# Performance work log

Hardware: AMD Instinct MI355X
Metric: run time of the kernel (lower is better)

Reference implementation:

```python
import jax, jax.numpy as jnp
import numpy as np

B, L, D, H, OUT = 4, 2048, 1024, 8, 256
DH = D // H
EPS = 1e-12


def setup_inputs() -> dict:
    key = jax.random.key(0)
    ks = jax.random.split(key, 20)
    s = lambda fan_in: 1.0 / np.sqrt(fan_in)
    def lin(k, fin, fout):
        k1, k2 = jax.random.split(k)
        w = jax.random.uniform(k1, (fin, fout), jnp.float32, -s(fin), s(fin))
        b = jax.random.uniform(k2, (fout,), jnp.float32, -s(fin), s(fin))
        return w, b
    x = jax.random.normal(ks[0], (B, L, D), jnp.float32)
    wq, bq = lin(ks[1], D, D)
    wk, bk = lin(ks[2], D, D)
    wv, bv = lin(ks[3], D, D)
    gamma = jnp.ones((D,), jnp.float32)
    beta = jnp.zeros((D,), jnp.float32)
    wff, bff = lin(ks[4], D, D)
    wc1, bc1 = lin(ks[5], D, D)
    wc2, bc2 = lin(ks[6], D, 1)
    wl1, bl1 = lin(ks[7], L, L)
    wl2, bl2 = lin(ks[8], L, OUT)
    return dict(x=x, wq=wq, bq=bq, wk=wk, bk=bk, wv=wv, bv=bv,
                gamma=gamma, beta=beta, wff=wff, bff=bff,
                wc1=wc1, bc1=bc1, wc2=wc2, bc2=bc2,
                wl1=wl1, bl1=bl1, wl2=wl2, bl2=bl2)


def layernorm(x, gamma, beta):
    mean = x.mean(-1, keepdims=True)
    var = ((x - mean) ** 2).mean(-1, keepdims=True)  # biased variance
    return gamma * (x - mean) / jnp.sqrt(var + EPS) + beta


def reference(x, wq, bq, wk, bk, wv, bv, gamma, beta, wff, bff,
              wc1, bc1, wc2, bc2, wl1, bl1, wl2, bl2):
    # multi-head self-attention (dropout = identity at inference)
    q = (x @ wq + bq).reshape(B, L, H, DH)
    k = (x @ wk + bk).reshape(B, L, H, DH)
    v = (x @ wv + bv).reshape(B, L, H, DH)
    scores = jnp.einsum('bqhd,bkhd->bhqk', q, k) / np.sqrt(DH)
    attn = jax.nn.softmax(scores, axis=-1)                  # [B,H,L,L]
    ctx = jnp.einsum('bhqk,bkhd->bqhd', attn, v).reshape(B, L, D)
    h = layernorm(x + ctx, gamma, beta)
    # feedforward: Linear + ReLU (hidden = d_model), residual + same layernorm params
    ff = jax.nn.relu(h @ wff + bff)
    h = layernorm(h + ff, gamma, beta)
    # collapse d_model -> 1
    c = jax.nn.relu(h @ wc1 + bc1)
    c = jax.nn.relu(c @ wc2 + bc2)                          # [B,L,1]
    c = jnp.squeeze(c, axis=-1)                             # [B,L]
    # collapse length -> out_featuresize
    c = jax.nn.relu(c @ wl1 + bl1)
    out = c @ wl2 + bl2                                     # [B,OUT]
    return out
```

## Files before the change

### kernel.cpp

```cpp
#include <hip/hip_runtime.h>

typedef unsigned short u16;
typedef unsigned int u32;
typedef __attribute__((ext_vector_type(4))) float f32x4;
typedef __attribute__((ext_vector_type(8))) short short8;
typedef __attribute__((ext_vector_type(4))) u32 u32x4;
typedef __attribute__((ext_vector_type(4))) u16 u16x4;

#define BB 4
#define LL 2048
#define DD 1024
#define HH 8
#define DHH 128

__device__ __forceinline__ u16 f2b(float f) {
  u32 u = __builtin_bit_cast(u32, f);
  u += 0x7fffu + ((u >> 16) & 1u);
  return (u16)(u >> 16);
}
__device__ __forceinline__ float b2f(u16 h) {
  u32 u = ((u32)h) << 16;
  return __builtin_bit_cast(float, u);
}
__device__ __forceinline__ float exp2_fast(float x) {
  float r;
  asm("v_exp_f32 %0, %1" : "=v"(r) : "v"(x));
  return r;
}
__device__ __forceinline__ u32 packbf(float a, float b) {
  return (u32)f2b(a) | ((u32)f2b(b) << 16);
}
__device__ __forceinline__ u32 bperm(int srcLane, u32 v) {
  return (u32)__builtin_amdgcn_ds_bpermute(srcLane << 2, (int)v);
}

#define GLDS16(g, l)                                                          \
  __builtin_amdgcn_global_load_lds(                                           \
      (const __attribute__((address_space(1))) void*)(g),                     \
      (__attribute__((address_space(3))) void*)(l), 16, 0, 0)

#define MFMA_BF16 __builtin_amdgcn_mfma_f32_16x16x32_bf16

__global__ __launch_bounds__(256) void cvt_k(const float* __restrict__ X,
                                             u16* __restrict__ Xb, long n) {
  long i = ((long)blockIdx.x * 256 + threadIdx.x) * 4;
  if (i >= n) return;
  f32x4 v = *(const f32x4*)(X + i);
  u16x4 o;
#pragma unroll
  for (int k = 0; k < 4; k++) o[k] = f2b(v[k]);
  *(u16x4*)(Xb + i) = o;
}

__global__ __launch_bounds__(256) void tr5_k(
    const float* __restrict__ s0, const float* __restrict__ s1,
    const float* __restrict__ s2, const float* __restrict__ s3,
    const float* __restrict__ s4, u16* __restrict__ d0, u16* __restrict__ d1,
    u16* __restrict__ d2, u16* __restrict__ d3, u16* __restrict__ d4) {
  const float* W;
  u16* WT;
  switch (blockIdx.z) {
    case 0: W = s0; WT = d0; break;
    case 1: W = s1; WT = d1; break;
    case 2: W = s2; WT = d2; break;
    case 3: W = s3; WT = d3; break;
    default: W = s4; WT = d4; break;
  }
  __shared__ float tile[32][33];
  const int bx = blockIdx.x, by = blockIdx.y;
  const int tx = threadIdx.x & 31, ty = threadIdx.x >> 5;
#pragma unroll
  for (int i = 0; i < 4; i++)
    tile[ty + i * 8][tx] =
        W[(long)(by * 32 + ty + i * 8) * 1024 + bx * 32 + tx];
  __syncthreads();
#pragma unroll
  for (int i = 0; i < 4; i++)
    WT[(long)(bx * 32 + ty + i * 8) * 1024 + by * 32 + tx] =
        f2b(tile[tx][ty + i * 8]);
}

__global__ __launch_bounds__(256, 3) void qkv_k(
    const u16* __restrict__ A, const u16* __restrict__ QT,
    const u16* __restrict__ KT, const u16* __restrict__ VTw,
    const float* __restrict__ bq, const float* __restrict__ bk,
    const float* __restrict__ bv, float qscale, u16* __restrict__ Qo,
    u16* __restrict__ Ko, u16* __restrict__ Vo) {
  __shared__ u16 As[2][128 * 32];
  __shared__ u16 Bs[2][128 * 32];
  const int K = 1024;
  const int nwg = gridDim.x * gridDim.y;
  const int bid = blockIdx.x + blockIdx.y * gridDim.x;
  const int swz = (bid & 7) * (nwg >> 3) + (bid >> 3);
  const int bxi = swz % 24, byi = swz / 24;
  const int sector = bxi >> 3;
  const u16* BT = sector == 0 ? QT : (sector == 1 ? KT : VTw);
  const float* bias = sector == 0 ? bq : (sector == 1 ? bk : bv);
  const float scale = sector == 0 ? qscale : 1.f;
  const int t = threadIdx.x;
  const int l = t & 63, w = t >> 6;
  const int lr = l & 15, lg = l >> 4;
  const int wr = (w >> 1) * 64, wc = (w & 1) * 64;
  const long bm = (long)byi * 128, bn = (long)(bxi & 7) * 128;
  const int srow = l >> 2;
  const int scol = (l & 3) * 8;
  const u16* Ag0 = A + (bm + w * 32 + srow) * (long)K + scol;
  const u16* Ag1 = A + (bm + w * 32 + 16 + srow) * (long)K + scol;
  const u16* Bg0 = BT + (bn + w * 32 + srow) * (long)K + scol;
  const u16* Bg1 = BT + (bn + w * 32 + 16 + srow) * (long)K + scol;
  const int wo = w * 1024;
  f32x4 acc[4][4] = {};
  GLDS16(Ag0, &As[0][wo]);
  GLDS16(Ag1, &As[0][wo + 512]);
  GLDS16(Bg0, &Bs[0][wo]);
  GLDS16(Bg1, &Bs[0][wo + 512]);
  __syncthreads();
  int cur = 0;
  for (int k0 = 0; k0 < K; k0 += 32) {
    const int nxt = cur ^ 1;
    if (k0 + 32 < K) {
      GLDS16(Ag0 + k0 + 32, &As[nxt][wo]);
      GLDS16(Ag1 + k0 + 32, &As[nxt][wo + 512]);
      GLDS16(Bg0 + k0 + 32, &Bs[nxt][wo]);
      GLDS16(Bg1 + k0 + 32, &Bs[nxt][wo + 512]);
    }
    short8 af[4], bf[4];
#pragma unroll
    for (int i = 0; i < 4; i++)
      af[i] = *(const short8*)&As[cur][(wr + i * 16 + lr) * 32 + lg * 8];
#pragma unroll
    for (int i = 0; i < 4; i++)
      bf[i] = *(const short8*)&Bs[cur][(wc + i * 16 + lr) * 32 + lg * 8];
#pragma unroll
    for (int i = 0; i < 4; i++)
#pragma unroll
      for (int j = 0; j < 4; j++)
        acc[i][j] = MFMA_BF16(af[i], bf[j], acc[i][j], 0, 0, 0);
    __syncthreads();
    cur = nxt;
  }
#pragma unroll
  for (int i = 0; i < 4; i++)
#pragma unroll
    for (int j = 0; j < 4; j++) {
      long col = bn + wc + j * 16 + lr;
      float bvv = bias[col];
      if (sector == 2) {
        long row0 = bm + wr + i * 16 + lg * 4;
        long b = row0 >> 11, l0 = row0 & 2047;
        u16x4 ov;
#pragma unroll
        for (int r = 0; r < 4; r++) ov[r] = f2b(acc[i][j][r] + bvv);
        *(u16x4*)(Vo + (b * 1024 + col) * 2048 + l0) = ov;
      } else {
        u16* Out = sector == 0 ? Qo : Ko;
#pragma unroll
        for (int r = 0; r < 4; r++) {
          long row = bm + wr + i * 16 + lg * 4 + r;
          Out[row * 1024 + col] = f2b((acc[i][j][r] + bvv) * scale);
        }
      }
    }
}

template <bool RELU, int OMODE>
__global__ __launch_bounds__(256, 4) void gemm_k(
    const u16* __restrict__ A, const u16* __restrict__ BT,
    const float* __restrict__ bias, u16* __restrict__ Cb,
    const float* __restrict__ w2, float* __restrict__ cvec, int M, int N,
    int K) {
  __shared__ u16 As[2][64 * 32];
  __shared__ u16 Bs[2][128 * 32];
  const int nwg = gridDim.x * gridDim.y;
  const int bid = blockIdx.x + blockIdx.y * gridDim.x;
  const int swz = (bid & 7) * (nwg >> 3) + (bid >> 3);
  const int bxi = swz % gridDim.x, byi = swz / gridDim.x;
  const int t = threadIdx.x;
  const int l = t & 63, w = t >> 6;
  const int lr = l & 15, lg = l >> 4;
  const int wr = (w >> 1) * 32, wc = (w & 1) * 64;
  const long bm = (long)byi * 64, bn = (long)bxi * 128;
  const int srow = l >> 2;
  const int scol = (l & 3) * 8;
  const u16* Ag0 = A + (bm + w * 16 + srow) * (long)K + scol;
  const u16* Bg0 = BT + (bn + w * 32 + srow) * (long)K + scol;
  const u16* Bg1 = BT + (bn + w * 32 + 16 + srow) * (long)K + scol;
  const int woA = w * 512;
  const int woB = w * 1024;
  f32x4 acc[2][4] = {};
  GLDS16(Ag0, &As[0][woA]);
  GLDS16(Bg0, &Bs[0][woB]);
  GLDS16(Bg1, &Bs[0][woB + 512]);
  __syncthreads();
  int cur = 0;
  for (int k0 = 0; k0 < K; k0 += 32) {
    const int nxt = cur ^ 1;
    if (k0 + 32 < K) {
      GLDS16(Ag0 + k0 + 32, &As[nxt][woA]);
      GLDS16(Bg0 + k0 + 32, &Bs[nxt][woB]);
      GLDS16(Bg1 + k0 + 32, &Bs[nxt][woB + 512]);
    }
    short8 af[2], bf[4];
#pragma unroll
    for (int i = 0; i < 2; i++)
      af[i] = *(const short8*)&As[cur][(wr + i * 16 + lr) * 32 + lg * 8];
#pragma unroll
    for (int j = 0; j < 4; j++)
      bf[j] = *(const short8*)&Bs[cur][(wc + j * 16 + lr) * 32 + lg * 8];
#pragma unroll
    for (int i = 0; i < 2; i++)
#pragma unroll
      for (int j = 0; j < 4; j++)
        acc[i][j] = MFMA_BF16(af[i], bf[j], acc[i][j], 0, 0, 0);
    __syncthreads();
    cur = nxt;
  }
  if (OMODE == 3) {
    float bvj[4], w2j[4];
#pragma unroll
    for (int j = 0; j < 4; j++) {
      long col = bn + wc + j * 16 + lr;
      bvj[j] = bias[col];
      w2j[j] = w2[col];
    }
#pragma unroll
    for (int i = 0; i < 2; i++)
#pragma unroll
      for (int r = 0; r < 4; r++) {
        float a2 = 0.f;
#pragma unroll
        for (int j = 0; j < 4; j++)
          a2 += fmaxf(acc[i][j][r] + bvj[j], 0.f) * w2j[j];
        a2 += __shfl_xor(a2, 1, 64);
        a2 += __shfl_xor(a2, 2, 64);
        a2 += __shfl_xor(a2, 4, 64);
        a2 += __shfl_xor(a2, 8, 64);
        if (lr == 0) {
          long row = bm + wr + i * 16 + lg * 4 + r;
          atomicAdd(&cvec[row], a2);
        }
      }
  } else {
#pragma unroll
    for (int i = 0; i < 2; i++)
#pragma unroll
      for (int j = 0; j < 4; j++) {
        long col = bn + wc + j * 16 + lr;
        float bv = bias[col];
#pragma unroll
        for (int r = 0; r < 4; r++) {
          long row = bm + wr + i * 16 + lg * 4 + r;
          float v2 = acc[i][j][r] + bv;
          if (RELU) v2 = fmaxf(v2, 0.f);
          Cb[row * N + col] = f2b(v2);
        }
      }
  }
}

__global__ __launch_bounds__(256, 2) void flash_k(const u16* __restrict__ Q,
                                                  const u16* __restrict__ Kb,
                                                  const u16* __restrict__ VT,
                                                  u16* __restrict__ ctx) {
  __shared__ u16 Ks2[2][64 * 128];
  __shared__ u16 Vs2[2][128 * 64];
  const int nwg = gridDim.x * gridDim.y;
  const int bid = blockIdx.x + blockIdx.y * gridDim.x;
  const int swz = (bid & 7) * (nwg >> 3) + (bid >> 3);
  const int bxi = swz % gridDim.x, byi = swz / gridDim.x;
  const int t = threadIdx.x;
  const int l = t & 63, w = t >> 6;
  const int lr = l & 15, lg = l >> 4;
  const int b = byi >> 3, h = byi & 7;
  const long kbase = ((long)b * LL) * DD + h * DHH;
  const long vtbase = ((long)(b * 8 + h) * DHH) * LL;
  const int q0 = bxi * 128;

  short8 qf0[4], qf1[4];
  {
    const u16* qp0 = Q + kbase + (long)(q0 + w * 32 + lr) * DD + lg * 8;
    const u16* qp1 = qp0 + 16 * DD;
#pragma unroll
    for (int c = 0; c < 4; c++) {
      qf0[c] = *(const short8*)(qp0 + c * 32);
      qf1[c] = *(const short8*)(qp1 + c * 32);
    }
  }
  f32x4 oacc0[8] = {}, oacc1[8] = {};
  float mprev0 = -1e30f, mprev1 = -1e30f;
  float lsum0 = 0.f, lsum1 = 0.f;

  const u16* kg[4];
  const u16* vg[4];
  u16* kl[4];
  u16* vl[4];
#pragma unroll
  for (int i = 0; i < 4; i++) {
    int rk = w * 16 + 4 * i + (l >> 4);
    kg[i] = Kb + kbase + (long)rk * DD + ((l & 15) ^ (rk & 7)) * 8;
    kl[i] = &Ks2[0][(w * 16 + 4 * i) * 128];
    int rv = w * 32 + 8 * i + (l >> 3);
    vg[i] = VT + vtbase + (long)rv * LL + ((l & 7) ^ (rv & 7)) * 8;
    vl[i] = &Vs2[0][(w * 32 + 8 * i) * 64];
  }
#pragma unroll
  for (int i = 0; i < 4; i++) {
    GLDS16(kg[i], kl[i]);
    GLDS16(vg[i], vl[i]);
  }
  __syncthreads();

  int colk[4], colv[2];
#pragma unroll
  for (int c = 0; c < 4; c++) colk[c] = (((c * 4 + lg) ^ (lr & 7)) * 8);
#pragma unroll
  for (int kk = 0; kk < 2; kk++) colv[kk] = (((kk * 4 + lg) ^ (lr & 7)) * 8);

  const int NT = LL / 64;
  for (int it = 0; it < NT; ++it) {
    const int cur = it & 1;
    if (it + 1 < NT) {
      const int ko = (cur ^ 1) * (64 * 128);
      const int vo = (cur ^ 1) * (128 * 64);
#pragma unroll
      for (int i = 0; i < 4; i++) {
        kg[i] += 64 * DD;
        vg[i] += 64;
        GLDS16(kg[i], kl[i] + ko);
        GLDS16(vg[i], vl[i] + vo);
      }
    }
    const u16* Kc = &Ks2[cur][0];
    const u16* Vc = &Vs2[cur][0];

    f32x4 s0[4] = {}, s1[4] = {};
    __builtin_amdgcn_s_setprio(1);
#pragma unroll
    for (int jc = 0; jc < 4; jc++)
#pragma unroll
      for (int c = 0; c < 4; c++) {
        short8 kf = *(const short8*)&Kc[(jc * 16 + lr) * 128 + colk[c]];
        s0[jc] = MFMA_BF16(kf, qf0[c], s0[jc], 0, 0, 0);
        s1[jc] = MFMA_BF16(kf, qf1[c], s1[jc], 0, 0, 0);
      }
    __builtin_amdgcn_s_setprio(0);

    float mx0 = fmaxf(fmaxf(s0[0][0], s0[0][1]), fmaxf(s0[0][2], s0[0][3]));
    float mx1 = fmaxf(fmaxf(s1[0][0], s1[0][1]), fmaxf(s1[0][2], s1[0][3]));
#pragma unroll
    for (int jc = 1; jc < 4; jc++) {
      mx0 = fmaxf(mx0, fmaxf(fmaxf(s0[jc][0], s0[jc][1]),
                             fmaxf(s0[jc][2], s0[jc][3])));
      mx1 = fmaxf(mx1, fmaxf(fmaxf(s1[jc][0], s1[jc][1]),
                             fmaxf(s1[jc][2], s1[jc][3])));
    }
    mx0 = fmaxf(mx0, __shfl_xor(mx0, 16, 64));
    mx0 = fmaxf(mx0, __shfl_xor(mx0, 32, 64));
    mx1 = fmaxf(mx1, __shfl_xor(mx1, 16, 64));
    mx1 = fmaxf(mx1, __shfl_xor(mx1, 32, 64));

    if (__any((int)((mx0 > mprev0 + 8.f) || (mx1 > mprev1 + 8.f)))) {
      float mn0 = fmaxf(mprev0, mx0), mn1 = fmaxf(mprev1, mx1);
      float al0 = exp2_fast(mprev0 - mn0), al1 = exp2_fast(mprev1 - mn1);
      mprev0 = mn0;
      mprev1 = mn1;
      lsum0 *= al0;
      lsum1 *= al1;
      float ar0[4], ar1[4];
#pragma unroll
      for (int r = 0; r < 4; r++) {
        ar0[r] = __shfl(al0, lg * 4 + r, 64);
        ar1[r] = __shfl(al1, lg * 4 + r, 64);
      }
#pragma unroll
      for (int d8 = 0; d8 < 8; d8++)
#pragma unroll
        for (int r = 0; r < 4; r++) {
          oacc0[d8][r] *= ar0[r];
          oacc1[d8][r] *= ar1[r];
        }
    }

    u32 pk0[4][2], pk1[4][2];
    float la0 = 0.f, la1 = 0.f;
#pragma unroll
    for (int jc = 0; jc < 4; jc++) {
      float a0 = exp2_fast(s0[jc][0] - mprev0);
      float a1 = exp2_fast(s0[jc][1] - mprev0);
      float a2 = exp2_fast(s0[jc][2] - mprev0);
      float a3 = exp2_fast(s0[jc][3] - mprev0);
      la0 += (a0 + a1) + (a2 + a3);
      pk0[jc][0] = packbf(a0, a1);
      pk0[jc][1] = packbf(a2, a3);
      float b0 = exp2_fast(s1[jc][0] - mprev1);
      float b1 = exp2_fast(s1[jc][1] - mprev1);
      float b2 = exp2_fast(s1[jc][2] - mprev1);
      float b3 = exp2_fast(s1[jc][3] - mprev1);
      la1 += (b0 + b1) + (b2 + b3);
      pk1[jc][0] = packbf(b0, b1);
      pk1[jc][1] = packbf(b2, b3);
    }
    lsum0 += la0;
    lsum1 += la1;

    short8 pf0[2], pf1[2];
#pragma unroll
    for (int kk = 0; kk < 2; kk++) {
      u32x4 av0, av1;
#pragma unroll
      for (int m = 0; m < 4; m++) {
        int srcl = lr + ((((lg & 1) << 1) + (m >> 1)) << 4);
        u32 x0 = bperm(srcl, pk0[2 * kk][m & 1]);
        u32 x1 = bperm(srcl, pk0[2 * kk + 1][m & 1]);
        av0[m] = (lg >> 1) ? x1 : x0;
        u32 y0 = bperm(srcl, pk1[2 * kk][m & 1]);
        u32 y1 = bperm(srcl, pk1[2 * kk + 1][m & 1]);
        av1[m] = (lg >> 1) ? y1 : y0;
      }
      pf0[kk] = __builtin_bit_cast(short8, av0);
      pf1[kk] = __builtin_bit_cast(short8, av1);
    }

    __builtin_amdgcn_s_setprio(1);
#pragma unroll
    for (int kk = 0; kk < 2; kk++)
#pragma unroll
      for (int d8 = 0; d8 < 8; d8++) {
        short8 vf = *(const short8*)&Vc[(d8 * 16 + lr) * 64 + colv[kk]];
        oacc0[d8] = MFMA_BF16(pf0[kk], vf, oacc0[d8], 0, 0, 0);
        oacc1[d8] = MFMA_BF16(pf1[kk], vf, oacc1[d8], 0, 0, 0);
      }
    __builtin_amdgcn_s_setprio(0);
    __syncthreads();
  }

  lsum0 += __shfl_xor(lsum0, 16, 64);
  lsum0 += __shfl_xor(lsum0, 32, 64);
  lsum1 += __shfl_xor(lsum1, 16, 64);
  lsum1 += __shfl_xor(lsum1, 32, 64);
#pragma unroll
  for (int r = 0; r < 4; r++) {
    float inv0 = 1.f / __shfl(lsum0, lg * 4 + r, 64);
    float inv1 = 1.f / __shfl(lsum1, lg * 4 + r, 64);
    u16* cp0 = ctx + kbase + (long)(q0 + w * 32 + lg * 4 + r) * DD;
    u16* cp1 = cp0 + 16 * DD;
#pragma unroll
    for (int d8 = 0; d8 < 8; d8++) {
      cp0[d8 * 16 + lr] = f2b(oacc0[d8][r] * inv0);
      cp1[d8 * 16 + lr] = f2b(oacc1[d8][r] * inv1);
    }
  }
}

template <bool XB, bool RB>
__global__ __launch_bounds__(256) void ln_k(const void* __restrict__ Xp,
                                            const void* __restrict__ Rp,
                                            const float* __restrict__ gamma,
                                            const float* __restrict__ beta,
                                            u16* __restrict__ Hb) {
  const int row = blockIdx.x, t = threadIdx.x;
  const long off = (long)row * DD + t * 4;
  f32x4 v;
  if (XB) {
    u16x4 xv = *(const u16x4*)((const u16*)Xp + off);
#pragma unroll
    for (int i = 0; i < 4; i++) v[i] = b2f(xv[i]);
  } else {
    v = *(const f32x4*)((const float*)Xp + off);
  }
  if (RB) {
    u16x4 rv = *(const u16x4*)((const u16*)Rp + off);
#pragma unroll
    for (int i = 0; i < 4; i++) v[i] += b2f(rv[i]);
  } else {
    f32x4 rv = *(const f32x4*)((const float*)Rp + off);
#pragma unroll
    for (int i = 0; i < 4; i++) v[i] += rv[i];
  }
  float s = v[0] + v[1] + v[2] + v[3];
  float q = v[0] * v[0] + v[1] * v[1] + v[2] * v[2] + v[3] * v[3];
#pragma unroll
  for (int m = 32; m >= 1; m >>= 1) {
    s += __shfl_xor(s, m, 64);
    q += __shfl_xor(q, m, 64);
  }
  __shared__ float red[8];
  if ((t & 63) == 0) {
    red[t >> 6] = s;
    red[4 + (t >> 6)] = q;
  }
  __syncthreads();
  s = red[0] + red[1] + red[2] + red[3];
  q = red[4] + red[5] + red[6] + red[7];
  const float mean = s * (1.f / 1024.f);
  const float var = q * (1.f / 1024.f) - mean * mean;
  const float rstd = rsqrtf(var + 1e-12f);
  f32x4 g = *(const f32x4*)(gamma + t * 4);
  f32x4 be = *(const f32x4*)(beta + t * 4);
  u16x4 ob;
#pragma unroll
  for (int i = 0; i < 4; i++)
    ob[i] = f2b(g[i] * (v[i] - mean) * rstd + be[i]);
  *(u16x4*)(Hb + off) = ob;
}

template <bool BR>
__global__ __launch_bounds__(256) void smm_part(const float* __restrict__ Cin,
                                                const float* __restrict__ W,
                                                float* __restrict__ P, int Lr,
                                                int N, int SL,
                                                const float* __restrict__ b0) {
  const int j = blockIdx.x * 256 + threadIdx.x;
  const int l0 = blockIdx.y * SL;
  const float bb = BR ? b0[0] : 0.f;
  float a0 = 0, a1 = 0, a2 = 0, a3 = 0;
  for (int ll = l0; ll < l0 + SL; ll++) {
    float wv = W[(long)ll * N + j];
    float c0 = Cin[ll], c1 = Cin[Lr + ll], c2 = Cin[2 * Lr + ll],
          c3 = Cin[3 * Lr + ll];
    if (BR) {
      c0 = fmaxf(c0 + bb, 0.f);
      c1 = fmaxf(c1 + bb, 0.f);
      c2 = fmaxf(c2 + bb, 0.f);
      c3 = fmaxf(c3 + bb, 0.f);
    }
    a0 += c0 * wv;
    a1 += c1 * wv;
    a2 += c2 * wv;
    a3 += c3 * wv;
  }
  float* Pp = P + ((long)blockIdx.y * 4) * N + j;
  Pp[0] = a0;
  Pp[N] = a1;
  Pp[2 * N] = a2;
  Pp[3 * N] = a3;
}

template <bool RELU>
__global__ __launch_bounds__(256) void smm_red(const float* __restrict__ P,
                                               const float* __restrict__ bias,
                                               float* __restrict__ Out, int N,
                                               int S) {
  const int j = blockIdx.x * 256 + threadIdx.x;
#pragma unroll
  for (int b = 0; b < 4; b++) {
    float a = 0;
    for (int s = 0; s < S; s++) a += P[((long)s * 4 + b) * N + j];
    a += bias[j];
    if (RELU) a = fmaxf(a, 0.f);
    Out[(long)b * N + j] = a;
  }
}

extern "C" void kernel_launch(void* const* d_in, const int* in_sizes, int n_in,
                              void* d_out, int out_size, void* d_ws,
                              size_t ws_size, hipStream_t stream) {
  (void)in_sizes; (void)n_in; (void)out_size; (void)ws_size;
  const float* x = (const float*)d_in[0];
  const float* wq = (const float*)d_in[1];
  const float* bq = (const float*)d_in[2];
  const float* wk = (const float*)d_in[3];
  const float* bk = (const float*)d_in[4];
  const float* wv = (const float*)d_in[5];
  const float* bv = (const float*)d_in[6];
  const float* gamma = (const float*)d_in[7];
  const float* beta = (const float*)d_in[8];
  const float* wff = (const float*)d_in[9];
  const float* bff = (const float*)d_in[10];
  const float* wc1 = (const float*)d_in[11];
  const float* bc1 = (const float*)d_in[12];
  const float* wc2 = (const float*)d_in[13];
  const float* bc2 = (const float*)d_in[14];
  const float* wl1 = (const float*)d_in[15];
  const float* bl1 = (const float*)d_in[16];
  const float* wl2 = (const float*)d_in[17];
  const float* bl2 = (const float*)d_in[18];

  char* wsp = (char*)d_ws;
  size_t off = 0;
  auto take = [&](size_t bytes) -> char* {
    char* p = wsp + off;
    off += (bytes + 255) & ~(size_t)255;
    return p;
  };
  u16* xb = (u16*)take((size_t)8192 * 1024 * 2);
  u16* wqT = (u16*)take((size_t)1024 * 1024 * 2);
  u16* wkT = (u16*)take((size_t)1024 * 1024 * 2);
  u16* wvT = (u16*)take((size_t)1024 * 1024 * 2);
  u16* wffT = (u16*)take((size_t)1024 * 1024 * 2);
  u16* wc1T = (u16*)take((size_t)1024 * 1024 * 2);
  u16* qb = (u16*)take((size_t)8192 * 1024 * 2);
  u16* kbuf = (u16*)take((size_t)8192 * 1024 * 2);
  u16* vT = (u16*)take((size_t)8192 * 1024 * 2);
  u16* ctxb = (u16*)take((size_t)8192 * 1024 * 2);
  u16* h1b = (u16*)take((size_t)8192 * 1024 * 2);
  u16* ffb = (u16*)take((size_t)8192 * 1024 * 2);
  float* cvec = (float*)take(8192 * 4);
  float* c3 = (float*)take(8192 * 4);
  float* P1 = (float*)take((size_t)16 * 4 * 2048 * 4);
  float* P2 = (float*)take((size_t)16 * 4 * 256 * 4);
  u16* h2b = qb;

  cvt_k<<<8192, 256, 0, stream>>>(x, xb, (long)8192 * 1024);
  tr5_k<<<dim3(32, 32, 5), 256, 0, stream>>>(wq, wk, wv, wff, wc1, wqT, wkT,
                                             wvT, wffT, wc1T);

  qkv_k<<<dim3(24, 64), 256, 0, stream>>>(xb, wqT, wkT, wvT, bq, bk, bv,
                                          0.12751743f, qb, kbuf, vT);
  flash_k<<<dim3(16, 32), 256, 0, stream>>>(qb, kbuf, vT, ctxb);
  ln_k<true, true><<<8192, 256, 0, stream>>>(xb, ctxb, gamma, beta, h1b);
  dim3 gg(8, 128);
  gemm_k<true, 1><<<gg, 256, 0, stream>>>(h1b, wffT, bff, ffb, nullptr,
                                          nullptr, 8192, 1024, 1024);
  ln_k<true, true><<<8192, 256, 0, stream>>>(h1b, ffb, gamma, beta, h2b);
  hipMemsetAsync(cvec, 0, 8192 * sizeof(float), stream);
  gemm_k<true, 3><<<gg, 256, 0, stream>>>(h2b, wc1T, bc1, nullptr, wc2, cvec,
                                          8192, 1024, 1024);
  smm_part<true><<<dim3(8, 16), 256, 0, stream>>>(cvec, wl1, P1, 2048, 2048,
                                                  128, bc2);
  smm_red<true><<<8, 256, 0, stream>>>(P1, bl1, c3, 2048, 16);
  smm_part<false><<<dim3(1, 16), 256, 0, stream>>>(c3, wl2, P2, 2048, 256,
                                                   128, nullptr);
  smm_red<false><<<1, 256, 0, stream>>>(P2, bl2, (float*)d_out, 256, 16);
}
```

Before: 355.9 us.

## Share a 64x128 GEMM mainloop with K-step 64 and XOR-swizzled LDS

Result: slower. 365.3 us (+2.6%).

```diff
diff --git a/kernel.cpp b/kernel.cpp
--- a/kernel.cpp
+++ b/kernel.cpp
@@ -80,15 +80,86 @@
         f2b(tile[tx][ty + i * 8]);
 }
 
+__device__ __forceinline__ void g64_loop(const u16* __restrict__ A,
+                                         const u16* __restrict__ BT, long bm,
+                                         long bn, int K, u16* As, u16* Bs,
+                                         f32x4 (&acc)[2][4]) {
+  const int t = threadIdx.x;
+  const int l = t & 63, w = t >> 6;
+  const int lr = l & 15, lg = l >> 4;
+  const int wr = (w >> 1) * 32, wc = (w & 1) * 64;
+  const int srow = l >> 3;
+  const int sc = l & 7;
+  const int ASZ = 64 * 64, BSZ = 128 * 64;
+  const u16* ag[2];
+  u16* al[2];
+  const u16* bg[4];
+  u16* bl[4];
+#pragma unroll
+  for (int g = 0; g < 2; g++) {
+    int r = w * 16 + g * 8 + srow;
+    ag[g] = A + (bm + r) * (long)K + ((sc ^ (r & 7)) * 8);
+    al[g] = As + r * 64;
+  }
+#pragma unroll
+  for (int g = 0; g < 4; g++) {
+    int r = w * 32 + g * 8 + srow;
+    bg[g] = BT + (bn + r) * (long)K + ((sc ^ (r & 7)) * 8);
+    bl[g] = Bs + r * 64;
+  }
+#pragma unroll
+  for (int g = 0; g < 2; g++) GLDS16(ag[g], al[g]);
+#pragma unroll
+  for (int g = 0; g < 4; g++) GLDS16(bg[g], bl[g]);
+  __syncthreads();
+  int cur = 0;
+  for (int k0 = 0; k0 < K; k0 += 64) {
+    const int nxt = cur ^ 1;
+    if (k0 + 64 < K) {
+#pragma unroll
+      for (int g = 0; g < 2; g++) GLDS16(ag[g] + k0 + 64, al[g] + nxt * ASZ);
+#pragma unroll
+      for (int g = 0; g < 4; g++) GLDS16(bg[g] + k0 + 64, bl[g] + nxt * BSZ);
+    }
+    const u16* Ac = As + cur * ASZ;
+    const u16* Bc = Bs + cur * BSZ;
+    short8 af[2][2], bf[4][2];
+#pragma unroll
+    for (int i = 0; i < 2; i++) {
+      const int row = wr + i * 16 + lr;
+#pragma unroll
+      for (int ks = 0; ks < 2; ks++)
+        af[i][ks] =
+            *(const short8*)&Ac[row * 64 + (((lg + ks * 4) ^ (lr & 7)) * 8)];
+    }
+#pragma unroll
+    for (int j = 0; j < 4; j++) {
+      const int row = wc + j * 16 + lr;
+#pragma unroll
+      for (int ks = 0; ks < 2; ks++)
+        bf[j][ks] =
+            *(const short8*)&Bc[row * 64 + (((lg + ks * 4) ^ (lr & 7)) * 8)];
+    }
+#pragma unroll
+    for (int i = 0; i < 2; i++)
+#pragma unroll
+      for (int j = 0; j < 4; j++) {
+        acc[i][j] = MFMA_BF16(af[i][0], bf[j][0], acc[i][j], 0, 0, 0);
+        acc[i][j] = MFMA_BF16(af[i][1], bf[j][1], acc[i][j], 0, 0, 0);
+      }
+    __syncthreads();
+    cur = nxt;
+  }
+}
+
 __global__ __launch_bounds__(256, 3) void qkv_k(
     const u16* __restrict__ A, const u16* __restrict__ QT,
     const u16* __restrict__ KT, const u16* __restrict__ VTw,
     const float* __restrict__ bq, const float* __restrict__ bk,
     const float* __restrict__ bv, float qscale, u16* __restrict__ Qo,
     u16* __restrict__ Ko, u16* __restrict__ Vo) {
-  __shared__ u16 As[2][128 * 32];
-  __shared__ u16 Bs[2][128 * 32];
-  const int K = 1024;
+  __shared__ u16 As[2 * 64 * 64];
+  __shared__ u16 Bs[2 * 128 * 64];
   const int nwg = gridDim.x * gridDim.y;
   const int bid = blockIdx.x + blockIdx.y * gridDim.x;
   const int swz = (bid & 7) * (nwg >> 3) + (bid >> 3);
@@ -97,50 +168,16 @@
   const u16* BT = sector == 0 ? QT : (sector == 1 ? KT : VTw);
   const float* bias = sector == 0 ? bq : (sector == 1 ? bk : bv);
   const float scale = sector == 0 ? qscale : 1.f;
+  const long bm = (long)byi * 64, bn = (long)(bxi & 7) * 128;
+  f32x4 acc[2][4] = {};
+  g64_loop(A, BT, bm, bn, 1024, As, Bs, acc);
+
   const int t = threadIdx.x;
   const int l = t & 63, w = t >> 6;
   const int lr = l & 15, lg = l >> 4;
-  const int wr = (w >> 1) * 64, wc = (w & 1) * 64;
-  const long bm = (long)byi * 128, bn = (long)(bxi & 7) * 128;
-  const int srow = l >> 2;
-  const int scol = (l & 3) * 8;
-  const u16* Ag0 = A + (bm + w * 32 + srow) * (long)K + scol;
-  const u16* Ag1 = A + (bm + w * 32 + 16 + srow) * (long)K + scol;
-  const u16* Bg0 = BT + (bn + w * 32 + srow) * (long)K + scol;
-  const u16* Bg1 = BT + (bn + w * 32 + 16 + srow) * (long)K + scol;
-  const int wo = w * 1024;
-  f32x4 acc[4][4] = {};
-  GLDS16(Ag0, &As[0][wo]);
-  GLDS16(Ag1, &As[0][wo + 512]);
-  GLDS16(Bg0, &Bs[0][wo]);
-  GLDS16(Bg1, &Bs[0][wo + 512]);
-  __syncthreads();
-  int cur = 0;
-  for (int k0 = 0; k0 < K; k0 += 32) {
-    const int nxt = cur ^ 1;
-    if (k0 + 32 < K) {
-      GLDS16(Ag0 + k0 + 32, &As[nxt][wo]);
-      GLDS16(Ag1 + k0 + 32, &As[nxt][wo + 512]);
-      GLDS16(Bg0 + k0 + 32, &Bs[nxt][wo]);
-      GLDS16(Bg1 + k0 + 32, &Bs[nxt][wo + 512]);
-    }
-    short8 af[4], bf[4];
-#pragma unroll
-    for (int i = 0; i < 4; i++)
-      af[i] = *(const short8*)&As[cur][(wr + i * 16 + lr) * 32 + lg * 8];
-#pragma unroll
-    for (int i = 0; i < 4; i++)
-      bf[i] = *(const short8*)&Bs[cur][(wc + i * 16 + lr) * 32 + lg * 8];
-#pragma unroll
-    for (int i = 0; i < 4; i++)
-#pragma unroll
-      for (int j = 0; j < 4; j++)
-        acc[i][j] = MFMA_BF16(af[i], bf[j], acc[i][j], 0, 0, 0);
-    __syncthreads();
-    cur = nxt;
-  }
-#pragma unroll
-  for (int i = 0; i < 4; i++)
+  const int wr = (w >> 1) * 32, wc = (w & 1) * 64;
+#pragma unroll
+  for (int i = 0; i < 2; i++)
 #pragma unroll
     for (int j = 0; j < 4; j++) {
       long col = bn + wc + j * 16 + lr;
@@ -164,57 +201,25 @@
 }
 
 template <bool RELU, int OMODE>
-__global__ __launch_bounds__(256, 4) void gemm_k(
+__global__ __launch_bounds__(256, 3) void gemm_k(
     const u16* __restrict__ A, const u16* __restrict__ BT,
     const float* __restrict__ bias, u16* __restrict__ Cb,
     const float* __restrict__ w2, float* __restrict__ cvec, int M, int N,
     int K) {
-  __shared__ u16 As[2][64 * 32];
-  __shared__ u16 Bs[2][128 * 32];
+  __shared__ u16 As[2 * 64 * 64];
+  __shared__ u16 Bs[2 * 128 * 64];
   const int nwg = gridDim.x * gridDim.y;
   const int bid = blockIdx.x + blockIdx.y * gridDim.x;
   const int swz = (bid & 7) * (nwg >> 3) + (bid >> 3);
   const int bxi = swz % gridDim.x, byi = swz / gridDim.x;
+  const long bm = (long)byi * 64, bn = (long)bxi * 128;
+  f32x4 acc[2][4] = {};
+  g64_loop(A, BT, bm, bn, K, As, Bs, acc);
+
   const int t = threadIdx.x;
   const int l = t & 63, w = t >> 6;
   const int lr = l & 15, lg = l >> 4;
   const int wr = (w >> 1) * 32, wc = (w & 1) * 64;
-  const long bm = (long)byi * 64, bn = (long)bxi * 128;
-  const int srow = l >> 2;
-  const int scol = (l & 3) * 8;
-  const u16* Ag0 = A + (bm + w * 16 + srow) * (long)K + scol;
-  const u16* Bg0 = BT + (bn + w * 32 + srow) * (long)K + scol;
-  const u16* Bg1 = BT + (bn + w * 32 + 16 + srow) * (long)K + scol;
-  const int woA = w * 512;
-  const int woB = w * 1024;
-  f32x4 acc[2][4] = {};
-  GLDS16(Ag0, &As[0][woA]);
-  GLDS16(Bg0, &Bs[0][woB]);
-  GLDS16(Bg1, &Bs[0][woB + 512]);
-  __syncthreads();
-  int cur = 0;
-  for (int k0 = 0; k0 < K; k0 += 32) {
-    const int nxt = cur ^ 1;
-    if (k0 + 32 < K) {
-      GLDS16(Ag0 + k0 + 32, &As[nxt][woA]);
-      GLDS16(Bg0 + k0 + 32, &Bs[nxt][woB]);
-      GLDS16(Bg1 + k0 + 32, &Bs[nxt][woB + 512]);
-    }
-    short8 af[2], bf[4];
-#pragma unroll
-    for (int i = 0; i < 2; i++)
-      af[i] = *(const short8*)&As[cur][(wr + i * 16 + lr) * 32 + lg * 8];
-#pragma unroll
-    for (int j = 0; j < 4; j++)
-      bf[j] = *(const short8*)&Bs[cur][(wc + j * 16 + lr) * 32 + lg * 8];
-#pragma unroll
-    for (int i = 0; i < 2; i++)
-#pragma unroll
-      for (int j = 0; j < 4; j++)
-        acc[i][j] = MFMA_BF16(af[i], bf[j], acc[i][j], 0, 0, 0);
-    __syncthreads();
-    cur = nxt;
-  }
   if (OMODE == 3) {
     float bvj[4], w2j[4];
 #pragma unroll
@@ -605,8 +610,8 @@
   tr5_k<<<dim3(32, 32, 5), 256, 0, stream>>>(wq, wk, wv, wff, wc1, wqT, wkT,
                                              wvT, wffT, wc1T);
 
-  qkv_k<<<dim3(24, 64), 256, 0, stream>>>(xb, wqT, wkT, wvT, bq, bk, bv,
-                                          0.12751743f, qb, kbuf, vT);
+  qkv_k<<<dim3(24, 128), 256, 0, stream>>>(xb, wqT, wkT, wvT, bq, bk, bv,
+                                           0.12751743f, qb, kbuf, vT);
   flash_k<<<dim3(16, 32), 256, 0, stream>>>(qb, kbuf, vT, ctxb);
   ln_k<true, true><<<8192, 256, 0, stream>>>(xb, ctxb, gamma, beta, h1b);
   dim3 gg(8, 128);
```
